# Kernel optimization log

Hardware: AMD Instinct MI355X
Metric: run time of the kernel (lower is better)

Reference implementation:

```python
import jax, jax.numpy as jnp
import numpy as np

B, C, N = 4, 3, 8192

def setup_inputs() -> dict:
    key = jax.random.key(0)
    k1, k2, k3 = jax.random.split(key, 3)
    return {
        "registration_pred": jax.random.normal(k1, (B, C, N), dtype=jnp.float32),
        "registration_gt": jax.random.normal(k2, (B, C, N), dtype=jnp.float32),
        "coords": jax.random.normal(k3, (B, C, N), dtype=jnp.float32),
    }

def reference(registration_pred, registration_gt, coords):
    # point clouds: [B, N, 3]
    pc1 = jnp.transpose(coords + registration_gt, (0, 2, 1))   # gt cloud
    pc2 = jnp.transpose(coords + registration_pred, (0, 2, 1)) # generated cloud
    sq1 = jnp.sum(pc1 * pc1, axis=-1)  # [B, N]
    sq2 = jnp.sum(pc2 * pc2, axis=-1)  # [B, M]
    dist = (-2.0 * jnp.einsum('bnc,bmc->bnm', pc1, pc2)
            + sq1[:, :, None] + sq2[:, None, :])
    dist1 = jnp.min(dist, axis=-1)  # nearest gen point for each gt point [B, N]
    dist2 = jnp.min(dist, axis=1)   # nearest gt point for each gen point [B, M]
    return jnp.mean(jnp.sum(dist1, axis=1)) + jnp.mean(jnp.sum(dist2, axis=1))
```

## Files before the change

kernel.cpp:

```cpp
#include <hip/hip_runtime.h>
#include <cfloat>
#include <cstdint>

#define BB    4
#define NN    8192
#define NT    8
#define TPB   256
#define NTILE (NT*TPB)
#define NBQ   (NN/NTILE)
#define MSL   128
#define MS    (NN/MSL)
#define NPAIR (MSL/2)

__device__ __forceinline__ unsigned mapf(float f) {
    unsigned b = __float_as_uint(f);
    return b ^ ((unsigned)((int)b >> 31) | 0x80000000u);
}
__device__ __forceinline__ float unmapf(unsigned u) {
    unsigned b = u ^ (((u & 0x80000000u) != 0u) ? 0x80000000u : 0xFFFFFFFFu);
    return __uint_as_float(b);
}

__global__ __launch_bounds__(TPB) void chamfer_onepass_kernel(
    const float* __restrict__ pred, const float* __restrict__ gt,
    const float* __restrict__ coords, unsigned* __restrict__ ws)
{
    const int b  = blockIdx.y;
    const int nb = blockIdx.x & (NBQ - 1);
    const int ms = blockIdx.x >> 2;
    const size_t base = (size_t)b * 3 * NN;
    const float* gr = gt     + base;
    const float* pr = pred   + base;
    const float* cc = coords + base;

    __shared__ float4 tileE[NPAIR];
    __shared__ float4 tileO[NPAIR];
    __shared__ float  colmin[4][MSL];

    const int tid = threadIdx.x;

    if (tid < MSL) {
        int m   = ms * MSL + tid;
        float x = cc[m]        + pr[m];
        float y = cc[NN + m]   + pr[NN + m];
        float z = cc[2*NN + m] + pr[2*NN + m];
        float4 v = make_float4(-2.f*x, -2.f*y, -2.f*z, fmaf(x, x, fmaf(y, y, z*z)));
        if (tid & 1) tileO[tid >> 1] = v; else tileE[tid >> 1] = v;
    }
    for (int j = tid; j < 4 * MSL; j += TPB) (&colmin[0][0])[j] = FLT_MAX;

    float px[NT], py[NT], pz[NT], sqn[NT], mv[NT];
    const int n0 = nb * NTILE + tid;
    #pragma unroll
    for (int k = 0; k < NT; ++k) {
        int n   = n0 + k * TPB;
        float x = cc[n]        + gr[n];
        float y = cc[NN + n]   + gr[NN + n];
        float z = cc[2*NN + n] + gr[2*NN + n];
        px[k] = x; py[k] = y; pz[k] = z;
        sqn[k] = fmaf(x, x, fmaf(y, y, z*z));
        mv[k]  = FLT_MAX;
    }
    __syncthreads();

    const int lane = tid & 63;
    float* cm = colmin[tid >> 6];

    int jp = lane;
    for (int i = 0; i < NPAIR; ++i) {
        float4 a = tileE[jp];
        float4 c = tileO[jp];
        float d0[NT], d1[NT];
        #pragma unroll
        for (int k = 0; k < NT; ++k) {
            d0[k] = fmaf(px[k], a.x, fmaf(py[k], a.y, fmaf(pz[k], a.z, sqn[k] + a.w)));
            d1[k] = fmaf(px[k], c.x, fmaf(py[k], c.y, fmaf(pz[k], c.z, sqn[k] + c.w)));
            mv[k] = fminf(fminf(mv[k], d0[k]), d1[k]);
        }
        float c0 = fminf(fminf(d0[0], d0[1]), d0[2]);
        c0 = fminf(fminf(c0, d0[3]), d0[4]);
        c0 = fminf(fminf(c0, d0[5]), d0[6]);
        c0 = fminf(c0, d0[7]);
        float c1 = fminf(fminf(d1[0], d1[1]), d1[2]);
        c1 = fminf(fminf(c1, d1[3]), d1[4]);
        c1 = fminf(fminf(c1, d1[5]), d1[6]);
        c1 = fminf(c1, d1[7]);
        float2* slot = (float2*)&cm[2 * jp];
        float2 old = *slot;
        old.x = fminf(old.x, c0);
        old.y = fminf(old.y, c1);
        *slot = old;
        jp = (jp + 1) & (NPAIR - 1);
    }

    unsigned* wsrow = ws + (size_t)b * NN;
    #pragma unroll
    for (int k = 0; k < NT; ++k)
        atomicMin(&wsrow[n0 + k * TPB], mapf(mv[k]));

    __syncthreads();
    unsigned* wscol = ws + (size_t)BB * NN + (size_t)b * NN;
    if (tid < MSL) {
        float v = fminf(fminf(colmin[0][tid], colmin[1][tid]),
                        fminf(colmin[2][tid], colmin[3][tid]));
        atomicMin(&wscol[ms * MSL + tid], mapf(v));
    }
}

__global__ __launch_bounds__(256) void chamfer_reduce_a(
    const unsigned* __restrict__ ws, float* __restrict__ partial)
{
    int idx = blockIdx.x * 256 + threadIdx.x;
    const uint4* p = (const uint4*)ws;
    uint4 u = p[idx];
    float s = (unmapf(u.x) + unmapf(u.y)) + (unmapf(u.z) + unmapf(u.w));
    #pragma unroll
    for (int off = 32; off > 0; off >>= 1)
        s += __shfl_down(s, off);
    __shared__ float sm[4];
    if ((threadIdx.x & 63) == 0) sm[threadIdx.x >> 6] = s;
    __syncthreads();
    if (threadIdx.x == 0)
        partial[blockIdx.x] = (sm[0] + sm[1]) + (sm[2] + sm[3]);
}

__global__ __launch_bounds__(64) void chamfer_reduce_b(
    const float* __restrict__ partial, float* __restrict__ out)
{
    float s = partial[threadIdx.x];
    #pragma unroll
    for (int off = 32; off > 0; off >>= 1)
        s += __shfl_down(s, off);
    if (threadIdx.x == 0) out[0] = s * (1.0f / (float)BB);
}

extern "C" void kernel_launch(void* const* d_in, const int* in_sizes, int n_in,
                              void* d_out, int out_size, void* d_ws, size_t ws_size,
                              hipStream_t stream) {
    const float* pred   = (const float*)d_in[0];
    const float* gt     = (const float*)d_in[1];
    const float* coords = (const float*)d_in[2];
    unsigned*    wsu    = (unsigned*)d_ws;
    float*       part   = (float*)((char*)d_ws + (size_t)2 * BB * NN * sizeof(unsigned));
    float*       out    = (float*)d_out;

    hipMemsetAsync(d_ws, 0xFF, (size_t)2 * BB * NN * sizeof(unsigned), stream);

    dim3 grid(NBQ * MS, BB);
    chamfer_onepass_kernel<<<grid, TPB, 0, stream>>>(pred, gt, coords, wsu);
    chamfer_reduce_a<<<64, 256, 0, stream>>>(wsu, part);
    chamfer_reduce_b<<<1, 64, 0, stream>>>(part, out);
}
```

Measured before the change: 44.13 us.

## Halve column slice, defer row norm add, prefetch tile, replace memset with kernel

The column slice shrinks from 128 to 64 points, which doubles the grid and makes each half-wave (32 lanes) own its own column-min row. The per-row squared norm is taken out of the inner FMA chain and added only once for the final row min and in the column-min reductions, and the next shared-memory tile entries are prefetched for the following iteration. The hipMemsetAsync is replaced by a small init kernel. Together these aim to cut inner-loop ALU work and launch overhead, at the cost of extra adds in the column reduction and more global atomics.

```diff
diff --git a/kernel.cpp b/kernel.cpp
--- a/kernel.cpp
+++ b/kernel.cpp
@@ -8,9 +8,10 @@
 #define TPB   256
 #define NTILE (NT*TPB)
 #define NBQ   (NN/NTILE)
-#define MSL   128
+#define MSL   64
 #define MS    (NN/MSL)
 #define NPAIR (MSL/2)
+#define NHW   (TPB/32)
 
 __device__ __forceinline__ unsigned mapf(float f) {
     unsigned b = __float_as_uint(f);
@@ -35,7 +36,7 @@
 
     __shared__ float4 tileE[NPAIR];
     __shared__ float4 tileO[NPAIR];
-    __shared__ float  colmin[4][MSL];
+    __shared__ float  colmin[NHW][MSL];
 
     const int tid = threadIdx.x;
 
@@ -47,7 +48,8 @@
         float4 v = make_float4(-2.f*x, -2.f*y, -2.f*z, fmaf(x, x, fmaf(y, y, z*z)));
         if (tid & 1) tileO[tid >> 1] = v; else tileE[tid >> 1] = v;
     }
-    for (int j = tid; j < 4 * MSL; j += TPB) (&colmin[0][0])[j] = FLT_MAX;
+    #pragma unroll
+    for (int j = tid; j < NHW * MSL; j += TPB) (&colmin[0][0])[j] = FLT_MAX;
 
     float px[NT], py[NT], pz[NT], sqn[NT], mv[NT];
     const int n0 = nb * NTILE + tid;
@@ -63,48 +65,58 @@
     }
     __syncthreads();
 
-    const int lane = tid & 63;
-    float* cm = colmin[tid >> 6];
+    const int ll = tid & 31;
+    float* cm = colmin[tid >> 5];
 
-    int jp = lane;
+    int jp = ll;
+    float4 a = tileE[jp];
+    float4 c = tileO[jp];
+    #pragma unroll 2
     for (int i = 0; i < NPAIR; ++i) {
-        float4 a = tileE[jp];
-        float4 c = tileO[jp];
+        const int jn = (jp + 1) & (NPAIR - 1);
+        float4 an = tileE[jn];
+        float4 cn = tileO[jn];
         float d0[NT], d1[NT];
         #pragma unroll
         for (int k = 0; k < NT; ++k) {
-            d0[k] = fmaf(px[k], a.x, fmaf(py[k], a.y, fmaf(pz[k], a.z, sqn[k] + a.w)));
-            d1[k] = fmaf(px[k], c.x, fmaf(py[k], c.y, fmaf(pz[k], c.z, sqn[k] + c.w)));
+            d0[k] = fmaf(px[k], a.x, fmaf(py[k], a.y, fmaf(pz[k], a.z, a.w)));
+            d1[k] = fmaf(px[k], c.x, fmaf(py[k], c.y, fmaf(pz[k], c.z, c.w)));
             mv[k] = fminf(fminf(mv[k], d0[k]), d1[k]);
         }
-        float c0 = fminf(fminf(d0[0], d0[1]), d0[2]);
-        c0 = fminf(fminf(c0, d0[3]), d0[4]);
-        c0 = fminf(fminf(c0, d0[5]), d0[6]);
-        c0 = fminf(c0, d0[7]);
-        float c1 = fminf(fminf(d1[0], d1[1]), d1[2]);
-        c1 = fminf(fminf(c1, d1[3]), d1[4]);
-        c1 = fminf(fminf(c1, d1[5]), d1[6]);
-        c1 = fminf(c1, d1[7]);
+        float c0 = fminf(fminf(d0[0] + sqn[0], d0[1] + sqn[1]), d0[2] + sqn[2]);
+        c0 = fminf(fminf(c0, d0[3] + sqn[3]), d0[4] + sqn[4]);
+        c0 = fminf(fminf(c0, d0[5] + sqn[5]), d0[6] + sqn[6]);
+        c0 = fminf(c0, d0[7] + sqn[7]);
+        float c1 = fminf(fminf(d1[0] + sqn[0], d1[1] + sqn[1]), d1[2] + sqn[2]);
+        c1 = fminf(fminf(c1, d1[3] + sqn[3]), d1[4] + sqn[4]);
+        c1 = fminf(fminf(c1, d1[5] + sqn[5]), d1[6] + sqn[6]);
+        c1 = fminf(c1, d1[7] + sqn[7]);
         float2* slot = (float2*)&cm[2 * jp];
         float2 old = *slot;
         old.x = fminf(old.x, c0);
         old.y = fminf(old.y, c1);
         *slot = old;
-        jp = (jp + 1) & (NPAIR - 1);
+        jp = jn; a = an; c = cn;
     }
 
     unsigned* wsrow = ws + (size_t)b * NN;
     #pragma unroll
     for (int k = 0; k < NT; ++k)
-        atomicMin(&wsrow[n0 + k * TPB], mapf(mv[k]));
+        atomicMin(&wsrow[n0 + k * TPB], mapf(mv[k] + sqn[k]));
 
     __syncthreads();
     unsigned* wscol = ws + (size_t)BB * NN + (size_t)b * NN;
     if (tid < MSL) {
-        float v = fminf(fminf(colmin[0][tid], colmin[1][tid]),
-                        fminf(colmin[2][tid], colmin[3][tid]));
+        float v = colmin[0][tid];
+        #pragma unroll
+        for (int h = 1; h < NHW; ++h) v = fminf(v, colmin[h][tid]);
         atomicMin(&wscol[ms * MSL + tid], mapf(v));
     }
+}
+
+__global__ __launch_bounds__(256) void ws_init_kernel(unsigned* __restrict__ ws)
+{
+    ((uint4*)ws)[blockIdx.x * 256 + threadIdx.x] = make_uint4(~0u, ~0u, ~0u, ~0u);
 }
 
 __global__ __launch_bounds__(256) void chamfer_reduce_a(
@@ -144,8 +156,7 @@
     float*       part   = (float*)((char*)d_ws + (size_t)2 * BB * NN * sizeof(unsigned));
     float*       out    = (float*)d_out;
 
-    hipMemsetAsync(d_ws, 0xFF, (size_t)2 * BB * NN * sizeof(unsigned), stream);
-
+    ws_init_kernel<<<64, 256, 0, stream>>>(wsu);
     dim3 grid(NBQ * MS, BB);
     chamfer_onepass_kernel<<<grid, TPB, 0, stream>>>(pred, gt, coords, wsu);
     chamfer_reduce_a<<<64, 256, 0, stream>>>(wsu, part);
```

Measured after the change: 43.32 us. Within noise of the previous version (-1.8%).
